# Kernel tuning notes

Measured on AMD Instinct MI355X. Metric: run time of the kernel, lower is better.

Reference implementation:

```python
import jax, jax.numpy as jnp
import numpy as np

EPS = 1e-3  # keras LayerNormalization default epsilon


def _layernorm(y, gamma, beta):
    m = jnp.mean(y, axis=-1, keepdims=True)
    v = jnp.var(y, axis=-1, keepdims=True)
    return (y - m) * jax.lax.rsqrt(v + EPS) * gamma + beta


def setup_inputs() -> dict:
    key = jax.random.key(0)
    ks = jax.random.split(key, 3)
    B, S, D, F = 4, 8192, 512, 2048
    x = jax.random.normal(ks[0], (B, S, D), dtype=jnp.float32)
    W1 = jax.random.normal(ks[1], (D, F), dtype=jnp.float32) * (1.0 / np.sqrt(D))
    b1 = jnp.zeros((F,), dtype=jnp.float32)
    W2 = jax.random.normal(ks[2], (F, D), dtype=jnp.float32) * (1.0 / np.sqrt(F))
    b2 = jnp.zeros((D,), dtype=jnp.float32)
    g1 = jnp.ones((D,), dtype=jnp.float32)
    be1 = jnp.zeros((D,), dtype=jnp.float32)
    g2 = jnp.ones((D,), dtype=jnp.float32)
    be2 = jnp.zeros((D,), dtype=jnp.float32)
    return {"x": x, "W1": W1, "b1": b1, "W2": W2, "b2": b2,
            "g1": g1, "be1": be1, "g2": g2, "be2": be2}


def reference(x, W1, b1, W2, b2, g1, be1, g2, be2):
    # 2D FFT over (seq, embed) axes; keep real part (FNet mixing)
    fft = jnp.real(jnp.fft.fft2(x.astype(jnp.complex64), axes=(-2, -1)))
    proj_input = _layernorm(x + fft, g1, be1)
    # FFN: Dense(dense_dim, relu) -> Dense(embed_dim)
    h = jax.nn.relu(jnp.einsum('bsd,df->bsf', proj_input, W1) + b1)
    proj_output = jnp.einsum('bsf,fd->bsd', h, W2) + b2
    return _layernorm(proj_input + proj_output, g2, be2)
```

## Files before the change

### kernel.cpp

```cpp
#include <hip/hip_runtime.h>

typedef unsigned short u16;
typedef unsigned int u32;
typedef short short8 __attribute__((ext_vector_type(8)));
typedef float f32x4 __attribute__((ext_vector_type(4)));

#define LN_EPS 1e-3f
#define PI2 6.28318530717958647692f
#define AS1 __attribute__((address_space(1)))
#define AS3 __attribute__((address_space(3)))

__device__ __forceinline__ u16 f2bf(float f) {
  u32 u = __float_as_uint(f);
  u += 0x7fffu + ((u >> 16) & 1u);
  return (u16)(u >> 16);
}
__device__ __forceinline__ float bf2f(u16 h) {
  return __uint_as_float(((u32)h) << 16);
}

__global__ __launch_bounds__(256) void prep_w(const float* __restrict__ W,
                                              u16* __restrict__ Wt, int R, int C) {
  __shared__ float tile[32][33];
  const int ct = C >> 5;
  int bc = blockIdx.x % ct;
  int br = blockIdx.x / ct;
  int tx = threadIdx.x & 31, ty = threadIdx.x >> 5;
  int r0 = br << 5, c0 = bc << 5;
#pragma unroll
  for (int i = 0; i < 32; i += 8)
    tile[ty + i][tx] = W[(size_t)(r0 + ty + i) * C + c0 + tx];
  __syncthreads();
#pragma unroll
  for (int i = 0; i < 32; i += 8)
    Wt[(size_t)(c0 + ty + i) * R + r0 + tx] = f2bf(tile[tx][ty + i]);
}

__global__ __launch_bounds__(256) void transpose_x(const float* __restrict__ x,
                                                   float* __restrict__ xt) {
  __shared__ float tile[32][33];
  int blk = blockIdx.x;
  int b = blk >> 12;
  int rem = blk & 4095;
  int st = rem >> 4;
  int dt = rem & 15;
  int tx = threadIdx.x & 31, ty = threadIdx.x >> 5;
  int s0 = st << 5, d0 = dt << 5;
#pragma unroll
  for (int i = 0; i < 32; i += 8)
    tile[ty + i][tx] = x[(((size_t)(b << 13) + s0 + ty + i) << 9) + d0 + tx];
  __syncthreads();
#pragma unroll
  for (int i = 0; i < 32; i += 8)
    xt[(((size_t)(b << 9) + d0 + ty + i) << 13) + s0 + tx] = tile[tx][ty + i];
}

__device__ __constant__ float C16r[8] = {1.f, 0.92387953f, 0.70710678f, 0.38268343f,
                                         0.f, -0.38268343f, -0.70710678f, -0.92387953f};
__device__ __constant__ float C16i[8] = {0.f, -0.38268343f, -0.70710678f, -0.92387953f,
                                         -1.f, -0.92387953f, -0.70710678f, -0.38268343f};
__device__ __constant__ float C8r[4] = {1.f, 0.70710678f, 0.f, -0.70710678f};
__device__ __constant__ float C8i[4] = {0.f, -0.70710678f, -1.f, -0.70710678f};
__device__ __constant__ float C4r[2] = {1.f, 0.f};
__device__ __constant__ float C4i[2] = {0.f, -1.f};
__device__ __constant__ float C32r[16] = {
    1.f, 0.98078528f, 0.92387953f, 0.83146961f, 0.70710678f, 0.55557023f,
    0.38268343f, 0.19509032f, 0.f, -0.19509032f, -0.38268343f, -0.55557023f,
    -0.70710678f, -0.83146961f, -0.92387953f, -0.98078528f};
__device__ __constant__ float C32i[16] = {
    0.f, -0.19509032f, -0.38268343f, -0.55557023f, -0.70710678f, -0.83146961f,
    -0.92387953f, -0.98078528f, -1.f, -0.98078528f, -0.92387953f, -0.83146961f,
    -0.70710678f, -0.55557023f, -0.38268343f, -0.19509032f};
__device__ __constant__ int REV4[16] = {0, 8, 4, 12, 2, 10, 6, 14,
                                        1, 9, 5, 13, 3, 11, 7, 15};

__device__ __forceinline__ constexpr int rev4c(int v) {
  return ((v & 1) << 3) | ((v & 2) << 1) | ((v & 4) >> 1) | ((v & 8) >> 3);
}

#define BFLY(ar, ai, br, bi, wr, wi)                 \
  {                                                  \
    float dr_ = (ar) - (br), di_ = (ai) - (bi);      \
    (ar) += (br);                                    \
    (ai) += (bi);                                    \
    (br) = dr_ * (wr)-di_ * (wi);                    \
    (bi) = dr_ * (wi) + di_ * (wr);                  \
  }

__global__ __launch_bounds__(512) void fft_s(float* __restrict__ X, float* __restrict__ Xim) {
  __shared__ float zr[8448], zi[8448];
  const int t = threadIdx.x;
  const int b = blockIdx.x >> 8;
  const int d0 = (blockIdx.x & 255) << 1;
  float* r0 = X + (((size_t)(b << 9) + d0) << 13);
  float* r1 = r0 + 8192;

  float xr[16], xi[16];
#pragma unroll
  for (int e = 0; e < 16; ++e) {
    xr[e] = r0[t + (e << 9)];
    xi[e] = r1[t + (e << 9)];
  }

  float c1, s1;
  sincosf(-PI2 * (float)t * (1.0f / 8192.0f), &s1, &c1);
  float c2 = c1 * c1 - s1 * s1, s2 = 2.f * c1 * s1;
  float c4 = c2 * c2 - s2 * s2, s4 = 2.f * c2 * s2;
  float c8 = c4 * c4 - s4 * s4, s8 = 2.f * c4 * s4;
#pragma unroll
  for (int e = 0; e < 8; ++e) {
    float wr = c1 * C16r[e] - s1 * C16i[e];
    float wi = c1 * C16i[e] + s1 * C16r[e];
    BFLY(xr[e], xi[e], xr[e + 8], xi[e + 8], wr, wi);
  }
#pragma unroll
  for (int e = 0; e < 16; ++e) {
    if ((e & 4) == 0) {
      int eb = e & 3;
      float wr = c2 * C8r[eb] - s2 * C8i[eb];
      float wi = c2 * C8i[eb] + s2 * C8r[eb];
      BFLY(xr[e], xi[e], xr[e + 4], xi[e + 4], wr, wi);
    }
  }
#pragma unroll
  for (int e = 0; e < 16; ++e) {
    if (((e >> 1) & 1) == 0) {
      int eb = e & 1;
      float wr = c4 * C4r[eb] - s4 * C4i[eb];
      float wi = c4 * C4i[eb] + s4 * C4r[eb];
      BFLY(xr[e], xi[e], xr[e + 2], xi[e + 2], wr, wi);
    }
  }
#pragma unroll
  for (int e = 0; e < 16; e += 2) {
    BFLY(xr[e], xi[e], xr[e + 1], xi[e + 1], c8, s8);
  }

#pragma unroll
  for (int e = 0; e < 16; ++e) {
    int idx = t + (e << 9);
    int a = idx + (idx >> 5);
    zr[a] = xr[e];
    zi[a] = xi[e];
  }
  __syncthreads();
  {
    const int f = t >> 5, l = t & 31;
#pragma unroll
    for (int e = 0; e < 16; ++e) {
      int idx = (f << 9) + (e << 5) + l;
      int a = idx + (idx >> 5);
      xr[e] = zr[a];
      xi[e] = zi[a];
    }
    float bc1, bs1;
    sincosf(-PI2 * (float)l * (1.0f / 512.0f), &bs1, &bc1);
    float bc2 = bc1 * bc1 - bs1 * bs1, bs2 = 2.f * bc1 * bs1;
    float bc4 = bc2 * bc2 - bs2 * bs2, bs4 = 2.f * bc2 * bs2;
    float bc8 = bc4 * bc4 - bs4 * bs4, bs8 = 2.f * bc4 * bs4;
#pragma unroll
    for (int e = 0; e < 8; ++e) {
      float wr = bc1 * C16r[e] - bs1 * C16i[e];
      float wi = bc1 * C16i[e] + bs1 * C16r[e];
      BFLY(xr[e], xi[e], xr[e + 8], xi[e + 8], wr, wi);
    }
#pragma unroll
    for (int e = 0; e < 16; ++e) {
      if (((e >> 2) & 1) == 0) {
        int eb = e & 3;
        float wr = bc2 * C8r[eb] - bs2 * C8i[eb];
        float wi = bc2 * C8i[eb] + bs2 * C8r[eb];
        BFLY(xr[e], xi[e], xr[e + 4], xi[e + 4], wr, wi);
      }
    }
#pragma unroll
    for (int e = 0; e < 16; ++e) {
      if (((e >> 1) & 1) == 0) {
        int eb = e & 1;
        float wr = bc4 * C4r[eb] - bs4 * C4i[eb];
        float wi = bc4 * C4i[eb] + bs4 * C4r[eb];
        BFLY(xr[e], xi[e], xr[e + 2], xi[e + 2], wr, wi);
      }
    }
#pragma unroll
    for (int e = 0; e < 16; e += 2) {
      BFLY(xr[e], xi[e], xr[e + 1], xi[e + 1], bc8, bs8);
    }
    __syncthreads();
#pragma unroll
    for (int e = 0; e < 16; ++e) {
      int idx = (f << 9) + (e << 5) + l;
      int a = idx + (idx >> 5);
      zr[a] = xr[e];
      zi[a] = xi[e];
    }
  }
  __syncthreads();
#pragma unroll
  for (int j = 0; j < 16; ++j) {
    int idx = (t << 4) + j;
    int a = idx + (idx >> 5);
    xr[j] = zr[a];
    xi[j] = zi[a];
  }

  {
    const int odd = t & 1;
#pragma unroll
    for (int j = 0; j < 16; ++j) {
      float pr = __shfl_xor(xr[j], 1);
      float pi = __shfl_xor(xi[j], 1);
      if (!odd) {
        xr[j] += pr;
        xi[j] += pi;
      } else {
        float dr = pr - xr[j], di = pi - xi[j];
        xr[j] = dr * C32r[j] - di * C32i[j];
        xi[j] = dr * C32i[j] + di * C32r[j];
      }
    }
#pragma unroll
    for (int j = 0; j < 8; ++j) {
      BFLY(xr[j], xi[j], xr[j + 8], xi[j + 8], C16r[j], C16i[j]);
    }
#pragma unroll
    for (int j = 0; j < 16; ++j) {
      if (((j >> 2) & 1) == 0) {
        BFLY(xr[j], xi[j], xr[j + 4], xi[j + 4], C8r[j & 3], C8i[j & 3]);
      }
    }
#pragma unroll
    for (int j = 0; j < 16; ++j) {
      if (((j >> 1) & 1) == 0) {
        BFLY(xr[j], xi[j], xr[j + 2], xi[j + 2], C4r[j & 1], C4i[j & 1]);
      }
    }
#pragma unroll
    for (int j = 0; j < 16; j += 2) {
      BFLY(xr[j], xi[j], xr[j + 1], xi[j + 1], 1.0f, 0.0f);
    }
  }

  __syncthreads();
  {
    const int rt = __brev((u32)t) >> 23;
#pragma unroll
    for (int j = 0; j < 16; ++j) {
      int k = (REV4[j] << 9) | rt;
      int a = k + (k >> 5);
      zr[a] = xr[j];
      zi[a] = xi[j];
    }
  }
  __syncthreads();

  float* i0 = Xim + (((size_t)(b << 9) + d0) << 13);
  float* i1 = i0 + 8192;
#pragma unroll
  for (int e = 0; e < 8; ++e) {
    int k = t + (e << 9);
    int nk = (8192 - k) & 8191;
    int ka = k + (k >> 5), na = nk + (nk >> 5);
    float zrk = zr[ka], zik = zi[ka], zrn = zr[na], zin = zi[na];
    r0[k] = 0.5f * (zrk + zrn);
    i0[k] = 0.5f * (zik - zin);
    r1[k] = 0.5f * (zik + zin);
    i1[k] = 0.5f * (zrn - zrk);
  }
  if (t == 0) {
    const int ka = 4096 + (4096 >> 5);
    float zrk = zr[ka], zik = zi[ka];
    r0[4096] = zrk;
    i0[4096] = 0.f;
    r1[4096] = zik;
    i1[4096] = 0.f;
  }
}

__global__ __launch_bounds__(256) void fft_d_ln(
    const float* __restrict__ Xre, const float* __restrict__ Xim,
    const float* __restrict__ x, const float* __restrict__ g1,
    const float* __restrict__ be1, u16* __restrict__ proj) {
  __shared__ float buf[16 * 528];
  const int tid = threadIdx.x;
  const int b = blockIdx.x / 257;
  const int kt = blockIdx.x - b * 257;
  const int s0 = kt << 4;
  const int row = tid >> 4, t = tid & 15;
  const int so = tid & 15, dd = tid >> 4;

  float xr[32], xi[32];

#pragma unroll
  for (int it = 0; it < 32; ++it) {
    int d = dd + (it << 4);
    buf[so * 516 + d] = Xre[(((size_t)(b << 9) + d) << 13) + s0 + so];
  }
  __syncthreads();
#pragma unroll
  for (int e = 0; e < 32; ++e) xr[e] = buf[row * 516 + t + (e << 4)];
  __syncthreads();
#pragma unroll
  for (int it = 0; it < 32; ++it) {
    int d = dd + (it << 4);
    buf[so * 516 + d] = Xim[(((size_t)(b << 9) + d) << 13) + s0 + so];
  }
  __syncthreads();
#pragma unroll
  for (int e = 0; e < 32; ++e) xi[e] = buf[row * 516 + t + (e << 4)];
  __syncthreads();

  float c1, s1;
  sincosf(-PI2 * (float)t * (1.0f / 512.0f), &s1, &c1);
  float c2 = c1 * c1 - s1 * s1, s2 = 2.f * c1 * s1;
  float c4 = c2 * c2 - s2 * s2, s4 = 2.f * c2 * s2;
  float c8 = c4 * c4 - s4 * s4, s8 = 2.f * c4 * s4;
  float c16 = c8 * c8 - s8 * s8, s16 = 2.f * c8 * s8;
#pragma unroll
  for (int e = 0; e < 16; ++e) {
    float wr = c1 * C32r[e] - s1 * C32i[e];
    float wi = c1 * C32i[e] + s1 * C32r[e];
    BFLY(xr[e], xi[e], xr[e + 16], xi[e + 16], wr, wi);
  }
#pragma unroll
  for (int e = 0; e < 32; ++e) {
    if ((e & 8) == 0) {
      int eb = e & 7;
      float wr = c2 * C16r[eb] - s2 * C16i[eb];
      float wi = c2 * C16i[eb] + s2 * C16r[eb];
      BFLY(xr[e], xi[e], xr[e + 8], xi[e + 8], wr, wi);
    }
  }
#pragma unroll
  for (int e = 0; e < 32; ++e) {
    if ((e & 4) == 0) {
      int eb = e & 3;
      float wr = c4 * C8r[eb] - s4 * C8i[eb];
      float wi = c4 * C8i[eb] + s4 * C8r[eb];
      BFLY(xr[e], xi[e], xr[e + 4], xi[e + 4], wr, wi);
    }
  }
#pragma unroll
  for (int e = 0; e < 32; ++e) {
    if ((e & 2) == 0) {
      int eb = e & 1;
      float wr = c8 * C4r[eb] - s8 * C4i[eb];
      float wi = c8 * C4i[eb] + s8 * C4r[eb];
      BFLY(xr[e], xi[e], xr[e + 2], xi[e + 2], wr, wi);
    }
  }
#pragma unroll
  for (int e = 0; e < 32; e += 2) {
    BFLY(xr[e], xi[e], xr[e + 1], xi[e + 1], c16, s16);
  }

#pragma unroll
  for (int e = 0; e < 32; ++e) {
    int p = (e << 4) + t;
    buf[row * 528 + p + (p >> 5)] = xr[e];
  }
  __syncthreads();
#pragma unroll
  for (int j = 0; j < 32; ++j) xr[j] = buf[row * 528 + 33 * t + j];
  __syncthreads();
#pragma unroll
  for (int e = 0; e < 32; ++e) {
    int p = (e << 4) + t;
    buf[row * 528 + p + (p >> 5)] = xi[e];
  }
  __syncthreads();
#pragma unroll
  for (int j = 0; j < 32; ++j) xi[j] = buf[row * 528 + 33 * t + j];
  __syncthreads();

#pragma unroll
  for (int o = 0; o < 32; o += 16) {
#pragma unroll
    for (int j = 0; j < 8; ++j)
      BFLY(xr[o + j], xi[o + j], xr[o + j + 8], xi[o + j + 8], C16r[j], C16i[j]);
#pragma unroll
    for (int j = 0; j < 16; ++j)
      if ((j & 4) == 0)
        BFLY(xr[o + j], xi[o + j], xr[o + j + 4], xi[o + j + 4], C8r[j & 3], C8i[j & 3]);
#pragma unroll
    for (int j = 0; j < 16; ++j)
      if ((j & 2) == 0)
        BFLY(xr[o + j], xi[o + j], xr[o + j + 2], xi[o + j + 2], C4r[j & 1], C4i[j & 1]);
#pragma unroll
    for (int j = 0; j < 16; j += 2)
      BFLY(xr[o + j], xi[o + j], xr[o + j + 1], xi[o + j + 1], 1.0f, 0.0f);
  }

  {
    const int rt4 = __brev((u32)t) >> 28;
#pragma unroll
    for (int j = 0; j < 16; ++j) {
      const int rj = rev4c(j);
      buf[row * 528 + 33 * rj + rt4] = xr[j];
      buf[row * 528 + 33 * rj + 16 + rt4] = xr[16 + j];
    }
  }
  __syncthreads();

  const int k = s0 + row;
  {
    const float* xrow = x + (((size_t)(b << 13) + k) << 9);
    float v[32];
    float sum = 0.f, sum2 = 0.f;
#pragma unroll
    for (int m = 0; m < 32; ++m) {
      int d = t + (m << 4);
      float val = buf[row * 528 + d + (d >> 5)] + xrow[d];
      v[m] = val;
      sum += val;
      sum2 += val * val;
    }
#pragma unroll
    for (int m = 1; m < 16; m <<= 1) {
      sum += __shfl_xor(sum, m, 16);
      sum2 += __shfl_xor(sum2, m, 16);
    }
    float mean = sum * (1.0f / 512.0f);
    float var = sum2 * (1.0f / 512.0f) - mean * mean;
    float scl = 1.0f / sqrtf(var + LN_EPS);
    if (k <= 4096) {
      u16* prow = proj + (((size_t)(b << 13) + k) << 9);
#pragma unroll
      for (int m = 0; m < 32; ++m) {
        int d = t + (m << 4);
        prow[d] = f2bf((v[m] - mean) * scl * g1[d] + be1[d]);
      }
    }
  }
  if (k >= 1 && k <= 4095) {
    const int sm = 8192 - k;
    const float* xrow = x + (((size_t)(b << 13) + sm) << 9);
    float v[32];
    float sum = 0.f, sum2 = 0.f;
#pragma unroll
    for (int m = 0; m < 32; ++m) {
      int d = t + (m << 4);
      int dm = (512 - d) & 511;
      float val = buf[row * 528 + dm + (dm >> 5)] + xrow[d];
      v[m] = val;
      sum += val;
      sum2 += val * val;
    }
#pragma unroll
    for (int m = 1; m < 16; m <<= 1) {
      sum += __shfl_xor(sum, m, 16);
      sum2 += __shfl_xor(sum2, m, 16);
    }
    float mean = sum * (1.0f / 512.0f);
    float var = sum2 * (1.0f / 512.0f) - mean * mean;
    float scl = 1.0f / sqrtf(var + LN_EPS);
    u16* prow = proj + (((size_t)(b << 13) + sm) << 9);
#pragma unroll
    for (int m = 0; m < 32; ++m) {
      int d = t + (m << 4);
      prow[d] = f2bf((v[m] - mean) * scl * g1[d] + be1[d]);
    }
  }
}

template <bool RELU, bool OUT_BF16, int GH>
__global__ __launch_bounds__(256, 2) void gemm_bt(
    const u16* __restrict__ A, const u16* __restrict__ Bt,
    const float* __restrict__ bias, void* __restrict__ Cout,
    int M, int N, int K) {
  const int tid = threadIdx.x;
  const int lane = tid & 63;
  const int wave = tid >> 6;
  const int wm = wave >> 1, wn = wave & 1;
  const int llo = lane & 15, lhi = lane >> 4;

  const int nwg = gridDim.x;
  const int q = nwg >> 3;
  const int b2 = ((int)blockIdx.x & 7) * q + ((int)blockIdx.x >> 3);
  const int NT = N >> 7;
  const int GSZ = GH * NT;
  const int grp = b2 / GSZ;
  const int r = b2 - grp * GSZ;
  const int tn = r / GH;
  const int tm = grp * GH + (r - tn * GH);
  const int m0 = tm << 7, n0 = tn << 7;

  __shared__ short8 smem[2048];
  char* ldsA = (char*)&smem[0];
  char* ldsB = ldsA + 16384;

  f32x4 acc[4][4] = {};

  const int trow = tid >> 3;
  const int ksw = (((tid & 7) ^ (trow & 7)) << 3);
  const int wbase = wave << 10;
  const int swz = (llo & 7) << 4;

  const int KT = K >> 6;
  for (int kt = 0; kt < KT; ++kt) {
    const int k0 = (kt << 6) + ksw;
    __syncthreads();
#pragma unroll
    for (int r4 = 0; r4 < 4; ++r4) {
      const int grow = (r4 << 5) + trow;
      const u16* ga = A + (size_t)(m0 + grow) * K + k0;
      const u16* gb = Bt + (size_t)(n0 + grow) * K + k0;
      __builtin_amdgcn_global_load_lds((const AS1 void*)ga,
                                       (AS3 void*)(ldsA + (r4 << 12) + wbase), 16, 0, 0);
      __builtin_amdgcn_global_load_lds((const AS1 void*)gb,
                                       (AS3 void*)(ldsB + (r4 << 12) + wbase), 16, 0, 0);
    }
    __syncthreads();
#pragma unroll
    for (int kk = 0; kk < 2; ++kk) {
      const int cbx = ((kk << 6) | (lhi << 4)) ^ swz;
      short8 af[4], bfr[4];
#pragma unroll
      for (int mt = 0; mt < 4; ++mt)
        af[mt] = *(const short8*)(ldsA + (((wm << 6) + (mt << 4) + llo) << 7) + cbx);
#pragma unroll
      for (int nt = 0; nt < 4; ++nt)
        bfr[nt] = *(const short8*)(ldsB + (((wn << 6) + (nt << 4) + llo) << 7) + cbx);
#pragma unroll
      for (int mt = 0; mt < 4; ++mt)
#pragma unroll
        for (int nt = 0; nt < 4; ++nt)
          acc[mt][nt] =
              __builtin_amdgcn_mfma_f32_16x16x32_bf16(af[mt], bfr[nt], acc[mt][nt], 0, 0, 0);
    }
  }
#pragma unroll
  for (int nt = 0; nt < 4; ++nt) {
    const int col = n0 + (wn << 6) + (nt << 4) + llo;
    const float bv = bias[col];
#pragma unroll
    for (int mt = 0; mt < 4; ++mt) {
      const int rbase = m0 + (wm << 6) + (mt << 4) + (lhi << 2);
#pragma unroll
      for (int j = 0; j < 4; ++j) {
        float v = acc[mt][nt][j] + bv;
        if (RELU) v = fmaxf(v, 0.0f);
        if (OUT_BF16) ((u16*)Cout)[(size_t)(rbase + j) * N + col] = f2bf(v);
        else          ((float*)Cout)[(size_t)(rbase + j) * N + col] = v;
      }
    }
  }
}

template <bool RELU, bool OUT_BF16, int GH>
__global__ __launch_bounds__(512, 2) void gemm256(
    const u16* __restrict__ A, const u16* __restrict__ Bt,
    const float* __restrict__ bias, void* __restrict__ Cout,
    int M, int N, int K) {
  const int tid = threadIdx.x;
  const int lane = tid & 63;
  const int wave = tid >> 6;
  const int wm = wave >> 2;
  const int wn = wave & 3;
  const int llo = lane & 15, lhi = lane >> 4;

  const int nwg = gridDim.x;
  const int q = nwg >> 3;
  const int b2 = ((int)blockIdx.x & 7) * q + ((int)blockIdx.x >> 3);
  const int NT = N >> 8;
  const int GSZ = GH * NT;
  const int grp = b2 / GSZ;
  const int rr = b2 - grp * GSZ;
  const int tn = rr / GH;
  const int tm = grp * GH + (rr - tn * GH);
  const int m0 = tm << 8, n0 = tn << 8;

  __shared__ short8 smem[8192];
  char* ldsA = (char*)&smem[0];
  char* ldsB = ldsA + 65536;

  f32x4 acc[8][4] = {};

  const int trow = tid >> 3;
  const int ksw = ((tid & 7) ^ (trow & 7)) << 3;
  const int swz = (llo & 7) << 4;
  const int cb0 = (lhi << 4) ^ swz;
  const char* Ab0 = ldsA + wm * 16384 + llo * 128;
  const char* Bb0 = ldsB + (wn >> 1) * 16384 + (((wn & 1) << 6) + llo) * 128;

#define GLDS(g_, d_) __builtin_amdgcn_global_load_lds((const AS1 void*)(g_), (AS3 void*)(d_), 16, 0, 0)
#define STAGE_A(kt, hf) {                                                        \
    const u16* g_ = A + (size_t)(m0 + ((hf) << 7) + trow) * K + ((kt) << 6) + ksw; \
    char* d_ = ldsA + (((kt)&1) << 15) + ((hf) << 14) + tid * 16;                \
    GLDS(g_, d_); GLDS(g_ + ((size_t)64) * K, d_ + 8192); }
#define STAGE_B(kt, hf) {                                                        \
    const u16* g_ = Bt + (size_t)(n0 + ((hf) << 7) + trow) * K + ((kt) << 6) + ksw; \
    char* d_ = ldsB + (((kt)&1) << 15) + ((hf) << 14) + tid * 16;                \
    GLDS(g_, d_); GLDS(g_ + ((size_t)64) * K, d_ + 8192); }
#define BAR() { __builtin_amdgcn_sched_barrier(0); __builtin_amdgcn_s_barrier(); \
                __builtin_amdgcn_sched_barrier(0); }
#define VMW(n_) { asm volatile("s_waitcnt vmcnt(" #n_ ")" ::: "memory"); }

  const int KT = K >> 6;
  STAGE_A(0, 0); STAGE_A(0, 1); STAGE_B(0, 0); STAGE_B(0, 1);
  STAGE_B(1, 0); STAGE_B(1, 1);
  VMW(0);
  BAR();

  for (int t0 = 0; t0 < KT; t0 += 2) {
    const bool pf = (t0 + 2 < KT);
#pragma unroll
    for (int s = 0; s < 2; ++s) {
      const char* Abase = Ab0 + (s << 15);
      const char* Bbase = Bb0 + (s << 15);
      short8 bfr[4][2];
      {
#pragma unroll
        for (int fn = 0; fn < 4; ++fn) {
          bfr[fn][0] = *(const short8*)(Bbase + fn * 2048 + cb0);
          bfr[fn][1] = *(const short8*)(Bbase + fn * 2048 + (cb0 ^ 64));
        }
        short8 af[2][2];
#pragma unroll
        for (int i = 0; i < 2; ++i) {
          af[i][0] = *(const short8*)(Abase + i * 2048 + cb0);
          af[i][1] = *(const short8*)(Abase + i * 2048 + (cb0 ^ 64));
        }
        if (s == 0) {
          STAGE_A(t0 + 1, 0); STAGE_A(t0 + 1, 1);
        } else if (pf) {
          STAGE_A(t0 + 2, 0); STAGE_A(t0 + 2, 1);
        }
        BAR();
        __builtin_amdgcn_s_setprio(1);
#pragma unroll
        for (int i = 0; i < 2; ++i)
#pragma unroll
          for (int fn = 0; fn < 4; ++fn)
#pragma unroll
            for (int kk = 0; kk < 2; ++kk)
              acc[i][fn] = __builtin_amdgcn_mfma_f32_16x16x32_bf16(
                  af[i][kk], bfr[fn][kk], acc[i][fn], 0, 0, 0);
        __builtin_amdgcn_s_setprio(0);
        BAR();
      }
#pragma unroll
      for (int qq = 1; qq < 4; ++qq) {
        short8 af[2][2];
#pragma unroll
        for (int i = 0; i < 2; ++i) {
          af[i][0] = *(const short8*)(Abase + (qq * 2 + i) * 2048 + cb0);
          af[i][1] = *(const short8*)(Abase + (qq * 2 + i) * 2048 + (cb0 ^ 64));
        }
        if (pf) {
          if (s == 0) {
            if (qq == 1) STAGE_B(t0 + 2, 0);
            if (qq == 2) STAGE_B(t0 + 2, 1);
          } else {
            if (qq == 1) STAGE_B(t0 + 3, 0);
            if (qq == 2) STAGE_B(t0 + 3, 1);
          }
        }
        BAR();
        __builtin_amdgcn_s_setprio(1);
#pragma unroll
        for (int i = 0; i < 2; ++i)
#pragma unroll
          for (int fn = 0; fn < 4; ++fn)
#pragma unroll
            for (int kk = 0; kk < 2; ++kk)
              acc[qq * 2 + i][fn] = __builtin_amdgcn_mfma_f32_16x16x32_bf16(
                  af[i][kk], bfr[fn][kk], acc[qq * 2 + i][fn], 0, 0, 0);
        __builtin_amdgcn_s_setprio(0);
        if (qq == 3) VMW(4);
        BAR();
      }
    }
  }
#undef GLDS
#undef STAGE_A
#undef STAGE_B
#undef BAR
#undef VMW

  float bv[4];
#pragma unroll
  for (int fn = 0; fn < 4; ++fn) bv[fn] = bias[n0 + (wn << 6) + (fn << 4) + llo];
#pragma unroll
  for (int fm = 0; fm < 8; ++fm) {
#pragma unroll
    for (int j = 0; j < 4; ++j) {
      const size_t row = (size_t)(m0 + (wm << 7) + (fm << 4) + (lhi << 2) + j);
#pragma unroll
      for (int fn = 0; fn < 4; ++fn) {
        const int col = n0 + (wn << 6) + (fn << 4) + llo;
        float v = acc[fm][fn][j] + bv[fn];
        if (RELU) v = fmaxf(v, 0.0f);
        if (OUT_BF16) ((u16*)Cout)[row * N + col] = f2bf(v);
        else          ((float*)Cout)[row * N + col] = v;
      }
    }
  }
}

__global__ __launch_bounds__(256) void ln2_kernel(
    float* __restrict__ out, const u16* __restrict__ proj,
    const float* __restrict__ g2, const float* __restrict__ be2) {
  const int lane = threadIdx.x & 63;
  const int row = blockIdx.x * 4 + (threadIdx.x >> 6);
  float* orow = out + ((size_t)row << 9);
  const u16* prow = proj + ((size_t)row << 9);
  const int d0 = lane << 3;
  f32x4 a0 = *(const f32x4*)(orow + d0);
  f32x4 a1 = *(const f32x4*)(orow + d0 + 4);
  short8 p = *(const short8*)(prow + d0);
  float y[8];
  float sum = 0.f, sum2 = 0.f;
#pragma unroll
  for (int m = 0; m < 8; ++m) {
    float v = (m < 4 ? a0[m] : a1[m - 4]) + bf2f((u16)p[m]);
    y[m] = v; sum += v; sum2 += v * v;
  }
#pragma unroll
  for (int m = 1; m < 64; m <<= 1) {
    sum += __shfl_xor(sum, m, 64);
    sum2 += __shfl_xor(sum2, m, 64);
  }
  float mean = sum * (1.0f / 512.0f);
  float var = sum2 * (1.0f / 512.0f) - mean * mean;
  float scl = 1.0f / sqrtf(var + LN_EPS);
  f32x4 g0 = *(const f32x4*)(g2 + d0);
  f32x4 g1v = *(const f32x4*)(g2 + d0 + 4);
  f32x4 e0 = *(const f32x4*)(be2 + d0);
  f32x4 e1 = *(const f32x4*)(be2 + d0 + 4);
  f32x4 o0, o1;
#pragma unroll
  for (int m = 0; m < 4; ++m) o0[m] = (y[m] - mean) * scl * g0[m] + e0[m];
#pragma unroll
  for (int m = 0; m < 4; ++m) o1[m] = (y[m + 4] - mean) * scl * g1v[m] + e1[m];
  *(f32x4*)(orow + d0) = o0;
  *(f32x4*)(orow + d0 + 4) = o1;
}

extern "C" void kernel_launch(void* const* d_in, const int* in_sizes, int n_in,
                              void* d_out, int out_size, void* d_ws, size_t ws_size,
                              hipStream_t stream) {
  const float* x   = (const float*)d_in[0];
  const float* W1  = (const float*)d_in[1];
  const float* b1  = (const float*)d_in[2];
  const float* W2  = (const float*)d_in[3];
  const float* b2  = (const float*)d_in[4];
  const float* g1  = (const float*)d_in[5];
  const float* be1 = (const float*)d_in[6];
  const float* g2  = (const float*)d_in[7];
  const float* be2 = (const float*)d_in[8];

  char* ws = (char*)d_ws;
  float* xre  = (float*)(ws);
  float* xim  = (float*)(ws + (64u << 20));
  u16*   proj = (u16*)(ws + (128u << 20));
  u16*   w1t  = (u16*)(ws + (160u << 20));
  u16*   w2t  = (u16*)(ws + (162u << 20));
  u16*   h    = (u16*)(ws);

  prep_w<<<1024, 256, 0, stream>>>(W1, w1t, 512, 2048);
  prep_w<<<1024, 256, 0, stream>>>(W2, w2t, 2048, 512);
  transpose_x<<<16384, 256, 0, stream>>>(x, xre);
  fft_s<<<1024, 512, 0, stream>>>(xre, xim);
  fft_d_ln<<<1028, 256, 0, stream>>>(xre, xim, x, g1, be1, proj);
  gemm_bt<true, true, 8><<<4096, 256, 0, stream>>>(proj, w1t, b1, (void*)h, 32768, 2048, 512);
  gemm256<false, false, 2><<<256, 512, 0, stream>>>(h, w2t, b2, d_out, 32768, 512, 2048);
  ln2_kernel<<<8192, 256, 0, stream>>>((float*)d_out, proj, g2, be2);
  (void)in_sizes; (void)n_in; (void)out_size; (void)ws_size;
}
```

Measured before the change: 280.2 us.

## Store FFT intermediates in bf16 and fuse residual add into second GEMM epilogue

The transposed input and the intermediate real/imaginary FFT buffers move from fp32 to bf16, halving the memory traffic of the transpose, the sequence FFT and the embed-dim FFT/LN kernels. The second GEMM now adds its result onto the bf16 proj buffer in place and writes bf16. The final layernorm then reads one bf16 tensor instead of an fp32 output plus the bf16 proj. This trades accuracy, since the FFT inputs and outputs and the pre-LN residual sum are rounded to bf16, for less bandwidth in several memory-bound stages.

```diff
diff --git a/kernel.cpp b/kernel.cpp
--- a/kernel.cpp
+++ b/kernel.cpp
@@ -37,7 +37,7 @@
 }
 
 __global__ __launch_bounds__(256) void transpose_x(const float* __restrict__ x,
-                                                   float* __restrict__ xt) {
+                                                   u16* __restrict__ xt) {
   __shared__ float tile[32][33];
   int blk = blockIdx.x;
   int b = blk >> 12;
@@ -52,7 +52,7 @@
   __syncthreads();
 #pragma unroll
   for (int i = 0; i < 32; i += 8)
-    xt[(((size_t)(b << 9) + d0 + ty + i) << 13) + s0 + tx] = tile[tx][ty + i];
+    xt[(((size_t)(b << 9) + d0 + ty + i) << 13) + s0 + tx] = f2bf(tile[tx][ty + i]);
 }
 
 __device__ __constant__ float C16r[8] = {1.f, 0.92387953f, 0.70710678f, 0.38268343f,
@@ -87,19 +87,19 @@
     (bi) = dr_ * (wi) + di_ * (wr);                  \
   }
 
-__global__ __launch_bounds__(512) void fft_s(float* __restrict__ X, float* __restrict__ Xim) {
+__global__ __launch_bounds__(512) void fft_s(u16* __restrict__ X, u16* __restrict__ Xim) {
   __shared__ float zr[8448], zi[8448];
   const int t = threadIdx.x;
   const int b = blockIdx.x >> 8;
   const int d0 = (blockIdx.x & 255) << 1;
-  float* r0 = X + (((size_t)(b << 9) + d0) << 13);
-  float* r1 = r0 + 8192;
+  u16* r0 = X + (((size_t)(b << 9) + d0) << 13);
+  u16* r1 = r0 + 8192;
 
   float xr[16], xi[16];
 #pragma unroll
   for (int e = 0; e < 16; ++e) {
-    xr[e] = r0[t + (e << 9)];
-    xi[e] = r1[t + (e << 9)];
+    xr[e] = bf2f(r0[t + (e << 9)]);
+    xi[e] = bf2f(r1[t + (e << 9)]);
   }
 
   float c1, s1;
@@ -254,31 +254,30 @@
   }
   __syncthreads();
 
-  float* i0 = Xim + (((size_t)(b << 9) + d0) << 13);
-  float* i1 = i0 + 8192;
+  u16* i0 = Xim + (((size_t)(b << 9) + d0) << 13);
+  u16* i1 = i0 + 8192;
 #pragma unroll
   for (int e = 0; e < 8; ++e) {
     int k = t + (e << 9);
     int nk = (8192 - k) & 8191;
     int ka = k + (k >> 5), na = nk + (nk >> 5);
     float zrk = zr[ka], zik = zi[ka], zrn = zr[na], zin = zi[na];
-    r0[k] = 0.5f * (zrk + zrn);
-    i0[k] = 0.5f * (zik - zin);
-    r1[k] = 0.5f * (zik + zin);
-    i1[k] = 0.5f * (zrn - zrk);
+    r0[k] = f2bf(0.5f * (zrk + zrn));
+    i0[k] = f2bf(0.5f * (zik - zin));
+    r1[k] = f2bf(0.5f * (zik + zin));
+    i1[k] = f2bf(0.5f * (zrn - zrk));
   }
   if (t == 0) {
     const int ka = 4096 + (4096 >> 5);
-    float zrk = zr[ka], zik = zi[ka];
-    r0[4096] = zrk;
-    i0[4096] = 0.f;
-    r1[4096] = zik;
-    i1[4096] = 0.f;
+    r0[4096] = f2bf(zr[ka]);
+    i0[4096] = 0;
+    r1[4096] = f2bf(zi[ka]);
+    i1[4096] = 0;
   }
 }
 
 __global__ __launch_bounds__(256) void fft_d_ln(
-    const float* __restrict__ Xre, const float* __restrict__ Xim,
+    const u16* __restrict__ Xre, const u16* __restrict__ Xim,
     const float* __restrict__ x, const float* __restrict__ g1,
     const float* __restrict__ be1, u16* __restrict__ proj) {
   __shared__ float buf[16 * 528];
@@ -294,7 +293,7 @@
 #pragma unroll
   for (int it = 0; it < 32; ++it) {
     int d = dd + (it << 4);
-    buf[so * 516 + d] = Xre[(((size_t)(b << 9) + d) << 13) + s0 + so];
+    buf[so * 516 + d] = bf2f(Xre[(((size_t)(b << 9) + d) << 13) + s0 + so]);
   }
   __syncthreads();
 #pragma unroll
@@ -303,7 +302,7 @@
 #pragma unroll
   for (int it = 0; it < 32; ++it) {
     int d = dd + (it << 4);
-    buf[so * 516 + d] = Xim[(((size_t)(b << 9) + d) << 13) + s0 + so];
+    buf[so * 516 + d] = bf2f(Xim[(((size_t)(b << 9) + d) << 13) + s0 + so]);
   }
   __syncthreads();
 #pragma unroll
@@ -547,7 +546,7 @@
   }
 }
 
-template <bool RELU, bool OUT_BF16, int GH>
+template <bool RELU, int OMODE, int GH>
 __global__ __launch_bounds__(512, 2) void gemm256(
     const u16* __restrict__ A, const u16* __restrict__ Bt,
     const float* __restrict__ bias, void* __restrict__ Cout,
@@ -691,30 +690,32 @@
         const int col = n0 + (wn << 6) + (fn << 4) + llo;
         float v = acc[fm][fn][j] + bv[fn];
         if (RELU) v = fmaxf(v, 0.0f);
-        if (OUT_BF16) ((u16*)Cout)[row * N + col] = f2bf(v);
-        else          ((float*)Cout)[row * N + col] = v;
+        if (OMODE == 2) {
+          u16* P = (u16*)Cout;
+          P[row * N + col] = f2bf(v + bf2f(P[row * N + col]));
+        } else {
+          ((u16*)Cout)[row * N + col] = f2bf(v);
+        }
       }
     }
   }
 }
 
 __global__ __launch_bounds__(256) void ln2_kernel(
-    float* __restrict__ out, const u16* __restrict__ proj,
+    float* __restrict__ out, const u16* __restrict__ y,
     const float* __restrict__ g2, const float* __restrict__ be2) {
   const int lane = threadIdx.x & 63;
   const int row = blockIdx.x * 4 + (threadIdx.x >> 6);
+  const u16* yrow = y + ((size_t)row << 9);
   float* orow = out + ((size_t)row << 9);
-  const u16* prow = proj + ((size_t)row << 9);
   const int d0 = lane << 3;
-  f32x4 a0 = *(const f32x4*)(orow + d0);
-  f32x4 a1 = *(const f32x4*)(orow + d0 + 4);
-  short8 p = *(const short8*)(prow + d0);
-  float y[8];
+  short8 p = *(const short8*)(yrow + d0);
+  float yv[8];
   float sum = 0.f, sum2 = 0.f;
 #pragma unroll
   for (int m = 0; m < 8; ++m) {
-    float v = (m < 4 ? a0[m] : a1[m - 4]) + bf2f((u16)p[m]);
-    y[m] = v; sum += v; sum2 += v * v;
+    float v = bf2f((u16)p[m]);
+    yv[m] = v; sum += v; sum2 += v * v;
   }
 #pragma unroll
   for (int m = 1; m < 64; m <<= 1) {
@@ -730,9 +731,9 @@
   f32x4 e1 = *(const f32x4*)(be2 + d0 + 4);
   f32x4 o0, o1;
 #pragma unroll
-  for (int m = 0; m < 4; ++m) o0[m] = (y[m] - mean) * scl * g0[m] + e0[m];
-#pragma unroll
-  for (int m = 0; m < 4; ++m) o1[m] = (y[m + 4] - mean) * scl * g1v[m] + e1[m];
+  for (int m = 0; m < 4; ++m) o0[m] = (yv[m] - mean) * scl * g0[m] + e0[m];
+#pragma unroll
+  for (int m = 0; m < 4; ++m) o1[m] = (yv[m + 4] - mean) * scl * g1v[m] + e1[m];
   *(f32x4*)(orow + d0) = o0;
   *(f32x4*)(orow + d0 + 4) = o1;
 }
@@ -751,20 +752,20 @@
   const float* be2 = (const float*)d_in[8];
 
   char* ws = (char*)d_ws;
-  float* xre  = (float*)(ws);
-  float* xim  = (float*)(ws + (64u << 20));
-  u16*   proj = (u16*)(ws + (128u << 20));
-  u16*   w1t  = (u16*)(ws + (160u << 20));
-  u16*   w2t  = (u16*)(ws + (162u << 20));
-  u16*   h    = (u16*)(ws);
+  u16* xt   = (u16*)(ws);
+  u16* xim  = (u16*)(ws + (32u << 20));
+  u16* proj = (u16*)(ws + (128u << 20));
+  u16* w1t  = (u16*)(ws + (160u << 20));
+  u16* w2t  = (u16*)(ws + (162u << 20));
+  u16* h    = (u16*)(ws);
 
   prep_w<<<1024, 256, 0, stream>>>(W1, w1t, 512, 2048);
   prep_w<<<1024, 256, 0, stream>>>(W2, w2t, 2048, 512);
-  transpose_x<<<16384, 256, 0, stream>>>(x, xre);
-  fft_s<<<1024, 512, 0, stream>>>(xre, xim);
-  fft_d_ln<<<1028, 256, 0, stream>>>(xre, xim, x, g1, be1, proj);
+  transpose_x<<<16384, 256, 0, stream>>>(x, xt);
+  fft_s<<<1024, 512, 0, stream>>>(xt, xim);
+  fft_d_ln<<<1028, 256, 0, stream>>>(xt, xim, x, g1, be1, proj);
   gemm_bt<true, true, 8><<<4096, 256, 0, stream>>>(proj, w1t, b1, (void*)h, 32768, 2048, 512);
-  gemm256<false, false, 2><<<256, 512, 0, stream>>>(h, w2t, b2, d_out, 32768, 512, 2048);
+  gemm256<false, 2, 2><<<256, 512, 0, stream>>>(h, w2t, b2, (void*)proj, 32768, 512, 2048);
   ln2_kernel<<<8192, 256, 0, stream>>>((float*)d_out, proj, g2, be2);
   (void)in_sizes; (void)n_in; (void)out_size; (void)ws_size;
 }
```

New measurement: 266.5 us. 4.9% less time.
